# Kernel tuning notes

Hardware: AMD Instinct MI355X
Metric: run time of the kernel (lower is better)

The kernel has to match this reference:

```python
import jax, jax.numpy as jnp
import numpy as np

N_NODES = 100000   # adj is [N, N], x is [N, D]
N_EDGES = 625000   # nnz of the COO adjacency
D_FEAT = 128       # embedding dim
EDGE_DROPOUT = 0.1


def setup_inputs() -> dict:
    key = jax.random.key(0)
    k1, k2, k3, k4 = jax.random.split(key, 4)
    x = jax.random.normal(k1, (N_NODES, D_FEAT), dtype=jnp.float32)
    edge_vals = jax.random.uniform(k2, (N_EDGES,), dtype=jnp.float32)
    edge_index = jax.random.randint(k3, (2, N_EDGES), 0, N_NODES)
    # training-mode edge dropout mask: keep edge iff u > edge_dropout
    keep_mask = jax.random.uniform(k4, (N_EDGES,)) > EDGE_DROPOUT
    return {"x": x, "edge_vals": edge_vals, "edge_index": edge_index, "keep_mask": keep_mask}


def reference(x, edge_vals, edge_index, keep_mask):
    # Dropping an edge from the COO tensor == zeroing its value in the SpMM.
    vals = jnp.where(keep_mask, edge_vals, jnp.zeros((), dtype=edge_vals.dtype))
    row = edge_index[0]  # destination rows of adj
    col = edge_index[1]  # source columns of adj
    # out[r] = sum_{e: row[e]==r} vals[e] * x[col[e]]   (torch.sparse.mm(adj, x))
    msgs = vals[:, None] * x[col]                      # [E, D]
    return jax.ops.segment_sum(msgs, row, num_segments=N_NODES)
```

## Files before the change

kernel.cpp:

```cpp
#include <hip/hip_runtime.h>

#define N_NODES 100000
#define N_EDGES 625000
#define D_FEAT  128

#define BKT_SHIFT 10
#define BKT_ROWS  1024
#define NBKT      ((N_NODES + BKT_ROWS - 1) / BKT_ROWS)
#define EPB       2048
#define ABLOCKS   ((N_EDGES + EPB - 1) / EPB)
#define CHCAP     48
#define CAPB      8192
#define CONV_BLOCKS (N_NODES * D_FEAT / 8 / 256)

#define BF_LO(u) __uint_as_float((u) << 16)
#define BF_HI(u) __uint_as_float((u) & 0xffff0000u)

__device__ __forceinline__ unsigned int rne_bf16(unsigned int u) {
    return (u + 0x7fffu + ((u >> 16) & 1u)) >> 16;
}

__global__ __launch_bounds__(256) void bucket_conv(
    const float* __restrict__ x, uint4* __restrict__ xb4,
    const int* __restrict__ ei, const int* __restrict__ keep,
    const float* __restrict__ vals,
    int*  __restrict__ counts,
    int2* __restrict__ chunks)
{
    int b = blockIdx.x;
    if (b < ABLOCKS) {
        __shared__ int cur[NBKT];
        int t = threadIdx.x;
        if (t < NBKT) cur[t] = 0;
        __syncthreads();
        int base = b * EPB;
        #pragma unroll
        for (int j = 0; j < 8; ++j) {
            int e = base + j * 256 + t;
            if (e < N_EDGES && keep[e]) {
                int r = ei[e];
                int bk = r >> BKT_SHIFT;
                int pos = atomicAdd(&cur[bk], 1);
                if (pos < CHCAP) {
                    int2 pr = { ei[N_EDGES + e] | ((r & (BKT_ROWS - 1)) << 17),
                                __float_as_int(vals[e]) };
                    chunks[((long long)b * NBKT + bk) * CHCAP + pos] = pr;
                }
            }
        }
        __syncthreads();
        if (t < NBKT) counts[b * NBKT + t] = min(cur[t], CHCAP);
    } else {
        int i = (b - ABLOCKS) * 256 + threadIdx.x;
        const float4* x4 = reinterpret_cast<const float4*>(x);
        float4 v0 = x4[i * 2], v1 = x4[i * 2 + 1];
        unsigned int a  = rne_bf16(__float_as_uint(v0.x));
        unsigned int bb = rne_bf16(__float_as_uint(v0.y));
        unsigned int c  = rne_bf16(__float_as_uint(v0.z));
        unsigned int d  = rne_bf16(__float_as_uint(v0.w));
        unsigned int e2 = rne_bf16(__float_as_uint(v1.x));
        unsigned int f  = rne_bf16(__float_as_uint(v1.y));
        unsigned int g  = rne_bf16(__float_as_uint(v1.z));
        unsigned int h  = rne_bf16(__float_as_uint(v1.w));
        uint4 o = { a | (bb << 16), c | (d << 16), e2 | (f << 16), g | (h << 16) };
        xb4[i] = o;
    }
}

__global__ __launch_bounds__(256) void build_csr(
    const int* __restrict__ counts, const int2* __restrict__ chunks,
    int2* __restrict__ fin, int2* __restrict__ rowinfo)
{
    __shared__ int2 ebuf[CAPB];
    __shared__ int  cbase[ABLOCKS + 1];
    __shared__ int  hist[BKT_ROWS];
    __shared__ int  ssum[256];
    int b = blockIdx.x, t = threadIdx.x;

    int i0 = 2 * t, i1 = 2 * t + 1;
    int c0 = (i0 < ABLOCKS) ? counts[i0 * NBKT + b] : 0;
    int c1 = (i1 < ABLOCKS) ? counts[i1 * NBKT + b] : 0;
    ssum[t] = c0 + c1;
    __syncthreads();
    for (int off = 1; off < 256; off <<= 1) {
        int add = (t >= off) ? ssum[t - off] : 0;
        __syncthreads();
        ssum[t] += add;
        __syncthreads();
    }
    int excl = (t == 0) ? 0 : ssum[t - 1];
    if (i0 < ABLOCKS) cbase[i0] = excl;
    if (i1 < ABLOCKS) cbase[i1] = excl + c0;
    if (t == 255) cbase[ABLOCKS] = ssum[255];
    __syncthreads();
    int ntot = cbase[ABLOCKS]; if (ntot > CAPB) ntot = CAPB;

    for (int c = t; c < ABLOCKS; c += 256) {
        int n = counts[c * NBKT + b];
        int cb = cbase[c];
        const int2* src = chunks + ((long long)c * NBKT + b) * CHCAP;
        for (int k = 0; k < n; ++k) {
            int dst = cb + k;
            if (dst < CAPB) ebuf[dst] = src[k];
        }
    }
    for (int i = t; i < BKT_ROWS; i += 256) hist[i] = 0;
    __syncthreads();

    for (int i = t; i < ntot; i += 256)
        atomicAdd(&hist[(ebuf[i].x >> 17) & (BKT_ROWS - 1)], 1);
    __syncthreads();

    int t4 = t * 4;
    int h0 = hist[t4], h1 = hist[t4 + 1], h2 = hist[t4 + 2], h3 = hist[t4 + 3];
    ssum[t] = h0 + h1 + h2 + h3;
    __syncthreads();
    for (int off = 1; off < 256; off <<= 1) {
        int add = (t >= off) ? ssum[t - off] : 0;
        __syncthreads();
        ssum[t] += add;
        __syncthreads();
    }
    int ex = (t == 0) ? 0 : ssum[t - 1];
    int s0 = ex, s1 = ex + h0, s2 = ex + h0 + h1, s3 = ex + h0 + h1 + h2;
    hist[t4] = s0; hist[t4 + 1] = s1; hist[t4 + 2] = s2; hist[t4 + 3] = s3;

    int rbase = b << BKT_SHIFT;
    int gbase = b * CAPB;
    int st[4] = { s0, s1, s2, s3 };
    int hh[4] = { h0, h1, h2, h3 };
    #pragma unroll
    for (int i = 0; i < 4; ++i) {
        int row = rbase + t4 + i;
        if (row < N_NODES) {
            int2 ri = { gbase + st[i], hh[i] };
            rowinfo[row] = ri;
        }
    }
    __syncthreads();

    for (int i = t; i < ntot; i += 256) {
        int2 pr = ebuf[i];
        int rl = (pr.x >> 17) & (BKT_ROWS - 1);
        int pos = atomicAdd(&hist[rl], 1);
        if (pos < CAPB) {
            int2 o = { pr.x & 0x1FFFF, pr.y };
            fin[gbase + pos] = o;
        }
    }
}

__global__ __launch_bounds__(256) void gather_csr_bf16(
    const uint4* __restrict__ xb4, const int2* __restrict__ rowinfo,
    const int2* __restrict__ fin, float4* __restrict__ out4)
{
    int gid = blockIdx.x * blockDim.x + threadIdx.x;
    int wave = gid >> 6;
    int lane = threadIdx.x & 63;
    int sub = lane >> 4, l16 = lane & 15;
    int row = wave * 4 + sub;
    if (row >= N_NODES) return;
    int2 ri = rowinfo[row];
    const int2* bp = fin + ri.x;
    int n = ri.y;

    float a0=0,a1=0,a2=0,a3=0,a4=0,a5=0,a6=0,a7=0;
    float c0=0,c1=0,c2=0,c3=0,c4=0,c5=0,c6=0,c7=0;
    int p = 0;
    for (; p + 2 <= n; p += 2) {
        int2 e0 = bp[p], e1 = bp[p + 1];
        uint4 g0 = xb4[(long long)e0.x * 16 + l16];
        uint4 g1 = xb4[(long long)e1.x * 16 + l16];
        float v0 = __int_as_float(e0.y), v1 = __int_as_float(e1.y);
        a0 += v0 * BF_LO(g0.x); a1 += v0 * BF_HI(g0.x);
        a2 += v0 * BF_LO(g0.y); a3 += v0 * BF_HI(g0.y);
        a4 += v0 * BF_LO(g0.z); a5 += v0 * BF_HI(g0.z);
        a6 += v0 * BF_LO(g0.w); a7 += v0 * BF_HI(g0.w);
        c0 += v1 * BF_LO(g1.x); c1 += v1 * BF_HI(g1.x);
        c2 += v1 * BF_LO(g1.y); c3 += v1 * BF_HI(g1.y);
        c4 += v1 * BF_LO(g1.z); c5 += v1 * BF_HI(g1.z);
        c6 += v1 * BF_LO(g1.w); c7 += v1 * BF_HI(g1.w);
    }
    if (p < n) {
        int2 e = bp[p];
        uint4 g = xb4[(long long)e.x * 16 + l16];
        float v = __int_as_float(e.y);
        a0 += v * BF_LO(g.x); a1 += v * BF_HI(g.x);
        a2 += v * BF_LO(g.y); a3 += v * BF_HI(g.y);
        a4 += v * BF_LO(g.z); a5 += v * BF_HI(g.z);
        a6 += v * BF_LO(g.w); a7 += v * BF_HI(g.w);
    }
    float4 o0 = { a0 + c0, a1 + c1, a2 + c2, a3 + c3 };
    float4 o1 = { a4 + c4, a5 + c5, a6 + c6, a7 + c7 };
    long long ob = (long long)row * 32 + l16 * 2;
    out4[ob]     = o0;
    out4[ob + 1] = o1;
}

__global__ __launch_bounds__(256) void gather_csr_f32(
    const float* __restrict__ x, const int2* __restrict__ rowinfo,
    const int2* __restrict__ fin, float* __restrict__ out)
{
    int gid = blockIdx.x * blockDim.x + threadIdx.x;
    int row = gid >> 6;
    if (row >= N_NODES) return;
    int lane = threadIdx.x & 63;
    int2 ri = rowinfo[row];
    const int2* bp = fin + ri.x;
    int n = ri.y;
    int d = lane * 2;
    float a0 = 0.f, b0 = 0.f, a1 = 0.f, b1 = 0.f;
    int p = 0;
    for (; p + 2 <= n; p += 2) {
        int2 e0 = bp[p], e1 = bp[p + 1];
        float2 x0 = *reinterpret_cast<const float2*>(x + (long long)e0.x * D_FEAT + d);
        float2 x1 = *reinterpret_cast<const float2*>(x + (long long)e1.x * D_FEAT + d);
        float v0 = __int_as_float(e0.y), v1 = __int_as_float(e1.y);
        a0 += v0 * x0.x; b0 += v0 * x0.y;
        a1 += v1 * x1.x; b1 += v1 * x1.y;
    }
    if (p < n) {
        int2 e = bp[p];
        float2 xv = *reinterpret_cast<const float2*>(x + (long long)e.x * D_FEAT + d);
        float v = __int_as_float(e.y);
        a0 += v * xv.x; b0 += v * xv.y;
    }
    float2 o = { a0 + a1, b0 + b1 };
    *reinterpret_cast<float2*>(out + (long long)row * D_FEAT + d) = o;
}

static inline size_t alignup(size_t v) { return (v + 511) / 512 * 512; }

extern "C" void kernel_launch(void* const* d_in, const int* in_sizes, int n_in,
                              void* d_out, int out_size, void* d_ws, size_t ws_size,
                              hipStream_t stream) {
    const float* x    = (const float*)d_in[0];
    const float* vals = (const float*)d_in[1];
    const int*   ei   = (const int*)d_in[2];
    const int*   keep = (const int*)d_in[3];
    float* out = (float*)d_out;

    const size_t sz_xb     = alignup((size_t)N_NODES * D_FEAT * 2);
    const size_t sz_counts = alignup((size_t)ABLOCKS * NBKT * 4);
    const size_t sz_chunks = alignup((size_t)ABLOCKS * NBKT * CHCAP * 8);
    const size_t sz_fin    = alignup((size_t)NBKT * CAPB * 8);
    const size_t sz_ri     = alignup((size_t)N_NODES * 8);
    const bool use_bf16 =
        ws_size >= sz_xb + sz_counts + sz_chunks + sz_fin + sz_ri;

    char* ws = (char*)d_ws;
    uint4* xb4 = nullptr;
    if (use_bf16) { xb4 = (uint4*)ws; ws += sz_xb; }
    int*  counts  = (int*)ws;   ws += sz_counts;
    int2* chunks  = (int2*)ws;  ws += sz_chunks;
    int2* fin     = (int2*)ws;  ws += sz_fin;
    int2* rowinfo = (int2*)ws;

    const int ablocks_total = use_bf16 ? (ABLOCKS + CONV_BLOCKS) : ABLOCKS;
    bucket_conv<<<ablocks_total, 256, 0, stream>>>(
        x, xb4, ei, keep, vals, counts, chunks);
    build_csr<<<NBKT, 256, 0, stream>>>(counts, chunks, fin, rowinfo);

    if (use_bf16) {
        const long long gthreads = (long long)((N_NODES + 3) / 4) * 64;
        gather_csr_bf16<<<(int)((gthreads + 255) / 256), 256, 0, stream>>>(
            xb4, rowinfo, fin, (float4*)out);
    } else {
        const long long gthreads = (long long)N_NODES * 64;
        gather_csr_f32<<<(int)((gthreads + 255) / 256), 256, 0, stream>>>(
            x, rowinfo, fin, out);
    }
}
```

Baseline: 72.93 us.

## Locally sort edges per block into dense buckets and unroll gather by four

The first pass now counting-sorts each block's kept edges by row bucket in shared memory. It writes them contiguously, with per-bucket offsets, instead of scattering them into fixed-capacity chunks of 48. build_csr reads the contiguous segments using the offset differences. This removes the chunk overflow cap and the sparse, poorly coalesced chunk writes, at the cost of an extra histogram and scan per block. Separately, the bf16 gather loop gains a 4-edge unrolled stage to put more loads in flight.

```diff
diff --git a/kernel.cpp b/kernel.cpp
--- a/kernel.cpp
+++ b/kernel.cpp
@@ -9,7 +9,7 @@
 #define NBKT      ((N_NODES + BKT_ROWS - 1) / BKT_ROWS)
 #define EPB       2048
 #define ABLOCKS   ((N_EDGES + EPB - 1) / EPB)
-#define CHCAP     48
+#define OSTRIDE   128
 #define CAPB      8192
 #define CONV_BLOCKS (N_NODES * D_FEAT / 8 / 256)
 
@@ -20,36 +20,61 @@
     return (u + 0x7fffu + ((u >> 16) & 1u)) >> 16;
 }
 
-__global__ __launch_bounds__(256) void bucket_conv(
+__global__ __launch_bounds__(256) void sort_conv(
     const float* __restrict__ x, uint4* __restrict__ xb4,
     const int* __restrict__ ei, const int* __restrict__ keep,
     const float* __restrict__ vals,
-    int*  __restrict__ counts,
-    int2* __restrict__ chunks)
+    int*  __restrict__ offs,
+    int2* __restrict__ dense)
 {
     int b = blockIdx.x;
     if (b < ABLOCKS) {
-        __shared__ int cur[NBKT];
+        __shared__ int2 ebuf[EPB];
+        __shared__ int  hist[128];
+        __shared__ int  scn[256];
+        __shared__ int  cur[128];
         int t = threadIdx.x;
-        if (t < NBKT) cur[t] = 0;
+        if (t < 128) hist[t] = 0;
         __syncthreads();
         int base = b * EPB;
+        int rows[8], cols[8]; float vv[8]; unsigned kmask = 0;
         #pragma unroll
         for (int j = 0; j < 8; ++j) {
             int e = base + j * 256 + t;
-            if (e < N_EDGES && keep[e]) {
-                int r = ei[e];
-                int bk = r >> BKT_SHIFT;
+            bool k = (e < N_EDGES) && (keep[e] != 0);
+            int r = 0, c = 0; float v = 0.f;
+            if (k) { r = ei[e]; c = ei[N_EDGES + e]; v = vals[e]; }
+            rows[j] = r; cols[j] = c; vv[j] = v;
+            if (k) { kmask |= (1u << j); atomicAdd(&hist[r >> BKT_SHIFT], 1); }
+        }
+        __syncthreads();
+        int v = (t < 128) ? hist[t] : 0;
+        scn[t] = v;
+        __syncthreads();
+        for (int off = 1; off < 256; off <<= 1) {
+            int add = (t >= off) ? scn[t - off] : 0;
+            __syncthreads();
+            scn[t] += add;
+            __syncthreads();
+        }
+        int excl = (t == 0) ? 0 : scn[t - 1];
+        if (t < 99) offs[b * OSTRIDE + t] = excl;
+        if (t < 128) cur[t] = excl;
+        __syncthreads();
+        #pragma unroll
+        for (int j = 0; j < 8; ++j) {
+            if (kmask & (1u << j)) {
+                int bk = rows[j] >> BKT_SHIFT;
                 int pos = atomicAdd(&cur[bk], 1);
-                if (pos < CHCAP) {
-                    int2 pr = { ei[N_EDGES + e] | ((r & (BKT_ROWS - 1)) << 17),
-                                __float_as_int(vals[e]) };
-                    chunks[((long long)b * NBKT + bk) * CHCAP + pos] = pr;
-                }
+                int2 pr = { cols[j] | ((rows[j] & (BKT_ROWS - 1)) << 17),
+                            __float_as_int(vv[j]) };
+                ebuf[pos] = pr;
             }
         }
         __syncthreads();
-        if (t < NBKT) counts[b * NBKT + t] = min(cur[t], CHCAP);
+        int nk = scn[127];
+        for (int i = t; i < nk; i += 256)
+            dense[(long long)b * EPB + i] = ebuf[i];
     } else {
         int i = (b - ABLOCKS) * 256 + threadIdx.x;
         const float4* x4 = reinterpret_cast<const float4*>(x);
@@ -68,7 +93,7 @@
 }
 
 __global__ __launch_bounds__(256) void build_csr(
-    const int* __restrict__ counts, const int2* __restrict__ chunks,
+    const int* __restrict__ offs, const int2* __restrict__ dense,
     int2* __restrict__ fin, int2* __restrict__ rowinfo)
 {
     __shared__ int2 ebuf[CAPB];
@@ -78,9 +103,10 @@
     int b = blockIdx.x, t = threadIdx.x;
 
     int i0 = 2 * t, i1 = 2 * t + 1;
-    int c0 = (i0 < ABLOCKS) ? counts[i0 * NBKT + b] : 0;
-    int c1 = (i1 < ABLOCKS) ? counts[i1 * NBKT + b] : 0;
-    ssum[t] = c0 + c1;
+    int l0 = 0, l1 = 0;
+    if (i0 < ABLOCKS) l0 = offs[i0 * OSTRIDE + b + 1] - offs[i0 * OSTRIDE + b];
+    if (i1 < ABLOCKS) l1 = offs[i1 * OSTRIDE + b + 1] - offs[i1 * OSTRIDE + b];
+    ssum[t] = l0 + l1;
     __syncthreads();
     for (int off = 1; off < 256; off <<= 1) {
         int add = (t >= off) ? ssum[t - off] : 0;
@@ -90,16 +116,17 @@
     }
     int excl = (t == 0) ? 0 : ssum[t - 1];
     if (i0 < ABLOCKS) cbase[i0] = excl;
-    if (i1 < ABLOCKS) cbase[i1] = excl + c0;
+    if (i1 < ABLOCKS) cbase[i1] = excl + l0;
     if (t == 255) cbase[ABLOCKS] = ssum[255];
     __syncthreads();
     int ntot = cbase[ABLOCKS]; if (ntot > CAPB) ntot = CAPB;
 
     for (int c = t; c < ABLOCKS; c += 256) {
-        int n = counts[c * NBKT + b];
+        int sstart = offs[c * OSTRIDE + b];
+        int len    = offs[c * OSTRIDE + b + 1] - sstart;
         int cb = cbase[c];
-        const int2* src = chunks + ((long long)c * NBKT + b) * CHCAP;
-        for (int k = 0; k < n; ++k) {
+        const int2* src = dense + (long long)c * EPB + sstart;
+        for (int k = 0; k < len; ++k) {
             int dst = cb + k;
             if (dst < CAPB) ebuf[dst] = src[k];
         }
@@ -167,6 +194,31 @@
     float a0=0,a1=0,a2=0,a3=0,a4=0,a5=0,a6=0,a7=0;
     float c0=0,c1=0,c2=0,c3=0,c4=0,c5=0,c6=0,c7=0;
     int p = 0;
+    for (; p + 4 <= n; p += 4) {
+        int2 e0 = bp[p], e1 = bp[p + 1], e2 = bp[p + 2], e3 = bp[p + 3];
+        uint4 g0 = xb4[(long long)e0.x * 16 + l16];
+        uint4 g1 = xb4[(long long)e1.x * 16 + l16];
+        uint4 g2 = xb4[(long long)e2.x * 16 + l16];
+        uint4 g3 = xb4[(long long)e3.x * 16 + l16];
+        float v0 = __int_as_float(e0.y), v1 = __int_as_float(e1.y);
+        float v2 = __int_as_float(e2.y), v3 = __int_as_float(e3.y);
+        a0 += v0 * BF_LO(g0.x); a1 += v0 * BF_HI(g0.x);
+        a2 += v0 * BF_LO(g0.y); a3 += v0 * BF_HI(g0.y);
+        a4 += v0 * BF_LO(g0.z); a5 += v0 * BF_HI(g0.z);
+        a6 += v0 * BF_LO(g0.w); a7 += v0 * BF_HI(g0.w);
+        c0 += v1 * BF_LO(g1.x); c1 += v1 * BF_HI(g1.x);
+        c2 += v1 * BF_LO(g1.y); c3 += v1 * BF_HI(g1.y);
+        c4 += v1 * BF_LO(g1.z); c5 += v1 * BF_HI(g1.z);
+        c6 += v1 * BF_LO(g1.w); c7 += v1 * BF_HI(g1.w);
+        a0 += v2 * BF_LO(g2.x); a1 += v2 * BF_HI(g2.x);
+        a2 += v2 * BF_LO(g2.y); a3 += v2 * BF_HI(g2.y);
+        a4 += v2 * BF_LO(g2.z); a5 += v2 * BF_HI(g2.z);
+        a6 += v2 * BF_LO(g2.w); a7 += v2 * BF_HI(g2.w);
+        c0 += v3 * BF_LO(g3.x); c1 += v3 * BF_HI(g3.x);
+        c2 += v3 * BF_LO(g3.y); c3 += v3 * BF_HI(g3.y);
+        c4 += v3 * BF_LO(g3.z); c5 += v3 * BF_HI(g3.z);
+        c6 += v3 * BF_LO(g3.w); c7 += v3 * BF_HI(g3.w);
+    }
     for (; p + 2 <= n; p += 2) {
         int2 e0 = bp[p], e1 = bp[p + 1];
         uint4 g0 = xb4[(long long)e0.x * 16 + l16];
@@ -240,26 +292,26 @@
     const int*   keep = (const int*)d_in[3];
     float* out = (float*)d_out;
 
-    const size_t sz_xb     = alignup((size_t)N_NODES * D_FEAT * 2);
-    const size_t sz_counts = alignup((size_t)ABLOCKS * NBKT * 4);
-    const size_t sz_chunks = alignup((size_t)ABLOCKS * NBKT * CHCAP * 8);
-    const size_t sz_fin    = alignup((size_t)NBKT * CAPB * 8);
-    const size_t sz_ri     = alignup((size_t)N_NODES * 8);
+    const size_t sz_xb    = alignup((size_t)N_NODES * D_FEAT * 2);
+    const size_t sz_offs  = alignup((size_t)ABLOCKS * OSTRIDE * 4);
+    const size_t sz_dense = alignup((size_t)ABLOCKS * EPB * 8);
+    const size_t sz_fin   = alignup((size_t)NBKT * CAPB * 8);
+    const size_t sz_ri    = alignup((size_t)N_NODES * 8);
     const bool use_bf16 =
-        ws_size >= sz_xb + sz_counts + sz_chunks + sz_fin + sz_ri;
+        ws_size >= sz_xb + sz_offs + sz_dense + sz_fin + sz_ri;
 
     char* ws = (char*)d_ws;
     uint4* xb4 = nullptr;
     if (use_bf16) { xb4 = (uint4*)ws; ws += sz_xb; }
-    int*  counts  = (int*)ws;   ws += sz_counts;
-    int2* chunks  = (int2*)ws;  ws += sz_chunks;
+    int*  offs    = (int*)ws;   ws += sz_offs;
+    int2* dense   = (int2*)ws;  ws += sz_dense;
     int2* fin     = (int2*)ws;  ws += sz_fin;
     int2* rowinfo = (int2*)ws;
 
     const int ablocks_total = use_bf16 ? (ABLOCKS + CONV_BLOCKS) : ABLOCKS;
-    bucket_conv<<<ablocks_total, 256, 0, stream>>>(
-        x, xb4, ei, keep, vals, counts, chunks);
-    build_csr<<<NBKT, 256, 0, stream>>>(counts, chunks, fin, rowinfo);
+    sort_conv<<<ablocks_total, 256, 0, stream>>>(
+        x, xb4, ei, keep, vals, offs, dense);
+    build_csr<<<NBKT, 256, 0, stream>>>(offs, dense, fin, rowinfo);
 
     if (use_bf16) {
         const long long gthreads = (long long)((N_NODES + 3) / 4) * 64;
```

New measurement: 81.45 us. 1.12x slower.

## Double bucket chunk size and software-prefetch edge indices in bf16 gather

Applied to the files above, without the earlier changes.

Each bucketing block now handles 4096 edges with a per-bucket chunk capacity of 80, which halves the number of chunk producers. build_csr can then map one thread per chunk, removing the two-per-thread scan and the strided copy loop. The bf16 gather loop now loads the next pair of edge descriptors before using the current ones, so index loads overlap with feature gathers. Larger chunks raise per-block atomic contention and use more scratch memory, and the overflow cap behaviour changes with the new CHCAP.

```diff
diff --git a/kernel.cpp b/kernel.cpp
--- a/kernel.cpp
+++ b/kernel.cpp
@@ -7,9 +7,9 @@
 #define BKT_SHIFT 10
 #define BKT_ROWS  1024
 #define NBKT      ((N_NODES + BKT_ROWS - 1) / BKT_ROWS)
-#define EPB       2048
+#define EPB       4096
 #define ABLOCKS   ((N_EDGES + EPB - 1) / EPB)
-#define CHCAP     48
+#define CHCAP     80
 #define CAPB      8192
 #define CONV_BLOCKS (N_NODES * D_FEAT / 8 / 256)
 
@@ -35,7 +35,7 @@
         __syncthreads();
         int base = b * EPB;
         #pragma unroll
-        for (int j = 0; j < 8; ++j) {
+        for (int j = 0; j < 16; ++j) {
             int e = base + j * 256 + t;
             if (e < N_EDGES && keep[e]) {
                 int r = ei[e];
@@ -77,10 +77,8 @@
     __shared__ int  ssum[256];
     int b = blockIdx.x, t = threadIdx.x;
 
-    int i0 = 2 * t, i1 = 2 * t + 1;
-    int c0 = (i0 < ABLOCKS) ? counts[i0 * NBKT + b] : 0;
-    int c1 = (i1 < ABLOCKS) ? counts[i1 * NBKT + b] : 0;
-    ssum[t] = c0 + c1;
+    int c0 = (t < ABLOCKS) ? counts[t * NBKT + b] : 0;
+    ssum[t] = c0;
     __syncthreads();
     for (int off = 1; off < 256; off <<= 1) {
         int add = (t >= off) ? ssum[t - off] : 0;
@@ -89,16 +87,15 @@
         __syncthreads();
     }
     int excl = (t == 0) ? 0 : ssum[t - 1];
-    if (i0 < ABLOCKS) cbase[i0] = excl;
-    if (i1 < ABLOCKS) cbase[i1] = excl + c0;
+    if (t < ABLOCKS) cbase[t] = excl;
     if (t == 255) cbase[ABLOCKS] = ssum[255];
     __syncthreads();
     int ntot = cbase[ABLOCKS]; if (ntot > CAPB) ntot = CAPB;
 
-    for (int c = t; c < ABLOCKS; c += 256) {
-        int n = counts[c * NBKT + b];
-        int cb = cbase[c];
-        const int2* src = chunks + ((long long)c * NBKT + b) * CHCAP;
+    if (t < ABLOCKS) {
+        int n  = counts[t * NBKT + b];
+        int cb = cbase[t];
+        const int2* src = chunks + ((long long)t * NBKT + b) * CHCAP;
         for (int k = 0; k < n; ++k) {
             int dst = cb + k;
             if (dst < CAPB) ebuf[dst] = src[k];
@@ -167,19 +164,37 @@
     float a0=0,a1=0,a2=0,a3=0,a4=0,a5=0,a6=0,a7=0;
     float c0=0,c1=0,c2=0,c3=0,c4=0,c5=0,c6=0,c7=0;
     int p = 0;
-    for (; p + 2 <= n; p += 2) {
-        int2 e0 = bp[p], e1 = bp[p + 1];
-        uint4 g0 = xb4[(long long)e0.x * 16 + l16];
-        uint4 g1 = xb4[(long long)e1.x * 16 + l16];
-        float v0 = __int_as_float(e0.y), v1 = __int_as_float(e1.y);
-        a0 += v0 * BF_LO(g0.x); a1 += v0 * BF_HI(g0.x);
-        a2 += v0 * BF_LO(g0.y); a3 += v0 * BF_HI(g0.y);
-        a4 += v0 * BF_LO(g0.z); a5 += v0 * BF_HI(g0.z);
-        a6 += v0 * BF_LO(g0.w); a7 += v0 * BF_HI(g0.w);
-        c0 += v1 * BF_LO(g1.x); c1 += v1 * BF_HI(g1.x);
-        c2 += v1 * BF_LO(g1.y); c3 += v1 * BF_HI(g1.y);
-        c4 += v1 * BF_LO(g1.z); c5 += v1 * BF_HI(g1.z);
-        c6 += v1 * BF_LO(g1.w); c7 += v1 * BF_HI(g1.w);
+    if (p + 2 <= n) {
+        int2 d0 = bp[0], d1 = bp[1];
+        for (; p + 4 <= n; p += 2) {
+            int2 nd0 = bp[p + 2], nd1 = bp[p + 3];
+            uint4 g0 = xb4[(long long)d0.x * 16 + l16];
+            uint4 g1 = xb4[(long long)d1.x * 16 + l16];
+            float v0 = __int_as_float(d0.y), v1 = __int_as_float(d1.y);
+            a0 += v0 * BF_LO(g0.x); a1 += v0 * BF_HI(g0.x);
+            a2 += v0 * BF_LO(g0.y); a3 += v0 * BF_HI(g0.y);
+            a4 += v0 * BF_LO(g0.z); a5 += v0 * BF_HI(g0.z);
+            a6 += v0 * BF_LO(g0.w); a7 += v0 * BF_HI(g0.w);
+            c0 += v1 * BF_LO(g1.x); c1 += v1 * BF_HI(g1.x);
+            c2 += v1 * BF_LO(g1.y); c3 += v1 * BF_HI(g1.y);
+            c4 += v1 * BF_LO(g1.z); c5 += v1 * BF_HI(g1.z);
+            c6 += v1 * BF_LO(g1.w); c7 += v1 * BF_HI(g1.w);
+            d0 = nd0; d1 = nd1;
+        }
+        {
+            uint4 g0 = xb4[(long long)d0.x * 16 + l16];
+            uint4 g1 = xb4[(long long)d1.x * 16 + l16];
+            float v0 = __int_as_float(d0.y), v1 = __int_as_float(d1.y);
+            a0 += v0 * BF_LO(g0.x); a1 += v0 * BF_HI(g0.x);
+            a2 += v0 * BF_LO(g0.y); a3 += v0 * BF_HI(g0.y);
+            a4 += v0 * BF_LO(g0.z); a5 += v0 * BF_HI(g0.z);
+            a6 += v0 * BF_LO(g0.w); a7 += v0 * BF_HI(g0.w);
+            c0 += v1 * BF_LO(g1.x); c1 += v1 * BF_HI(g1.x);
+            c2 += v1 * BF_LO(g1.y); c3 += v1 * BF_HI(g1.y);
+            c4 += v1 * BF_LO(g1.z); c5 += v1 * BF_HI(g1.z);
+            c6 += v1 * BF_LO(g1.w); c7 += v1 * BF_HI(g1.w);
+            p += 2;
+        }
     }
     if (p < n) {
         int2 e = bp[p];
```

After: 75.57 us. +3.6%, slower.
